# Performance work log

Hardware: AMD Instinct MI355X
Metric: run time of the kernel (lower is better)

The kernel has to match this reference:

```python
import jax, jax.numpy as jnp
import numpy as np

CONF_THRES = 0.8
NMS_THRES = 0.4
MAX_DET = 300          # fixed capacity for jit-compatible NMS output
N_BOXES = 262144
N_CLASSES = 80


def xywh2xyxy(x):
    xy, wh = x[..., :2], x[..., 2:4]
    return jnp.concatenate([xy - wh * 0.5, xy + wh * 0.5], axis=-1)


def bbox_iou(box, boxes):
    # one box [4] vs many [N,4]; original uses the +1 pixel-area convention
    x1 = jnp.maximum(box[0], boxes[:, 0])
    y1 = jnp.maximum(box[1], boxes[:, 1])
    x2 = jnp.minimum(box[2], boxes[:, 2])
    y2 = jnp.minimum(box[3], boxes[:, 3])
    inter = jnp.clip(x2 - x1 + 1, 0) * jnp.clip(y2 - y1 + 1, 0)
    a1 = (box[2] - box[0] + 1) * (box[3] - box[1] + 1)
    a2 = (boxes[:, 2] - boxes[:, 0] + 1) * (boxes[:, 3] - boxes[:, 1] + 1)
    return inter / (a1 + a2 - inter + 1e-16)


def nms_single(pred):
    # pred: [N, 85] raw YOLO output for one image
    boxes = xywh2xyxy(pred[:, :4])
    obj = pred[:, 4]
    cls_scores = pred[:, 5:]
    class_conf = cls_scores.max(axis=-1)
    class_pred = jnp.argmax(cls_scores, axis=-1).astype(pred.dtype)
    valid = obj >= CONF_THRES
    score = obj * class_conf
    # sort valid boxes by descending score; invalid pushed to the end
    order = jnp.argsort(jnp.where(valid, -score, jnp.inf))
    det = jnp.concatenate(
        [boxes, obj[:, None], class_conf[:, None], class_pred[:, None]], axis=1
    )[order]  # [N, 7] = x1,y1,x2,y2,obj,class_conf,class_pred
    valid = valid[order]

    def step(valid, _):
        idx = jnp.argmax(valid)            # first still-valid (= highest score)
        any_valid = jnp.any(valid)
        cur = det[idx]
        iou = bbox_iou(cur[:4], det[:, :4])
        invalid = (iou > NMS_THRES) & (det[:, 6] == cur[6]) & valid
        # weighted box merge over the suppressed group (as in original NMS)
        w = jnp.where(invalid, det[:, 4], 0.0)
        merged = (w[:, None] * det[:, :4]).sum(0) / (w.sum() + 1e-16)
        out = jnp.where(any_valid,
                        jnp.concatenate([merged, cur[4:]]),
                        jnp.zeros(7, pred.dtype))
        return valid & ~invalid, (out, any_valid)

    _, (kept, kept_valid) = jax.lax.scan(step, valid, None, length=MAX_DET)
    return kept, kept_valid  # [MAX_DET,7], [MAX_DET]


def setup_inputs() -> dict:
    key = jax.random.key(0)
    detections = jax.random.uniform(key, (1, N_BOXES, 5 + N_CLASSES), dtype=jnp.float32)
    return {"detections": detections}


def reference(detections):
    kept, kv = nms_single(detections[0])
    d = kept[:, 5:]                        # [MAX_DET, 2] = (class_conf, class_pred)
    conf_key = jnp.where(kv, d[:, 0], -jnp.inf)  # padded rows sort to the end
    order = jnp.argsort(conf_key)          # ascending (torch argsort)
    d = d[order][::-1]                     # torch.flip -> descending class_conf
    kv = kv[order][::-1]
    probs = jnp.where(kv, d[:, 0], 0.0)    # self.probs
    ids = d[:, 1][None, :]                 # self.ids, shape [1, MAX_DET]
    return ids, probs
```

## Files before the change

kernel.cpp:

```cpp
#include <hip/hip_runtime.h>

#pragma clang fp contract(off)

#define NBOX 262144
#define NCLS 80
#define ROWS 85
#define CAP 1024
#define NSUB 8
#define SUBCAP 128
#define POOL 8192
#define BPT 2
#define S1BOX 512

typedef unsigned long long ull;

__global__ __launch_bounds__(1024) void k_init(int* __restrict__ cnt_pad,
                                               int* __restrict__ pool_count) {
    const int t = threadIdx.x;
    for (int i = t; i < NCLS * NSUB * 16; i += 1024) cnt_pad[i] = 0;
    if (t == 0) *pool_count = 0;
}

__global__ __launch_bounds__(256) void k_stage1(const float* __restrict__ det,
                                                int* __restrict__ cnt_pad,
                                                ull* __restrict__ key2,
                                                float* __restrict__ conf2,
                                                float4* __restrict__ box2) {
    __shared__ int s_wl[S1BOX];
    __shared__ float s_obj[S1BOX];
    __shared__ int s_nv;
    const int t = threadIdx.x;
    const int b0 = blockIdx.x * S1BOX;
    const int sb = blockIdx.x & (NSUB - 1);

    if (t == 0) s_nv = 0;
    __syncthreads();

    float obj[BPT];
    #pragma unroll
    for (int i = 0; i < BPT; i++)
        obj[i] = det[(size_t)(b0 + (i << 8) + t) * ROWS + 4];
    #pragma unroll
    for (int i = 0; i < BPT; i++) {
        if (obj[i] >= 0.8f) {
            int r = atomicAdd(&s_nv, 1);
            s_wl[r] = (i << 8) + t;
            s_obj[r] = obj[i];
        }
    }
    __syncthreads();
    const int nv = s_nv;

    const int grp = t >> 4, c = t & 15;
    const int lane = t & 63;
    #pragma unroll 2
    for (int r0 = 0; r0 < nv; r0 += 16) {
        int widx = r0 + grp;
        if (widx < nv) {
            int b = s_wl[widx];
            const float* p = det + (size_t)(b0 + b) * ROWS;
            float aux = (c < 5) ? p[c] : 0.0f;
            float v0 = p[5 + c];
            float v1 = p[21 + c];
            float v2 = p[37 + c];
            float v3 = p[53 + c];
            float v4 = p[69 + c];
            float mv = v0; int mj = c;
            if (v1 > mv) { mv = v1; mj = 16 + c; }
            if (v2 > mv) { mv = v2; mj = 32 + c; }
            if (v3 > mv) { mv = v3; mj = 48 + c; }
            if (v4 > mv) { mv = v4; mj = 64 + c; }
            #pragma unroll
            for (int off = 8; off; off >>= 1) {
                float ov = __shfl_xor(mv, off);
                int oj = __shfl_xor(mj, off);
                if (ov > mv || (ov == mv && oj < mj)) { mv = ov; mj = oj; }
            }
            int gb = lane & 48;
            float x = __shfl(aux, gb + 0);
            float y = __shfl(aux, gb + 1);
            float w = __shfl(aux, gb + 2);
            float h = __shfl(aux, gb + 3);
            if (c == 0) {
                float ob = s_obj[widx];
                float score = ob * mv;
                float hw = w * 0.5f, hh = h * 0.5f;
                int gi = b0 + b;
                int r = atomicAdd(&cnt_pad[((mj * NSUB + sb) << 4)], 1);
                if (r < SUBCAP) {
                    int pos = (mj << 10) + (sb << 7) + r;
                    key2[pos] = ((ull)(~__float_as_uint(score)) << 32) | (unsigned)gi;
                    conf2[pos] = mv;
                    box2[pos] = make_float4(x - hw, y - hh, x + hw, y + hh);
                }
            }
        }
    }
}

template <int L>
__device__ __forceinline__ int exact_alive(ull (&k)[L]) {
    int a = 0;
    #pragma unroll
    for (int j = 0; j < L; j++) a += (int)__popcll(__ballot(k[j] != ~0ULL));
    return a;
}

template <int L>
__device__ __forceinline__ void pick_loop(ull (&k)[L], float4 (&bx)[L], float (&cf)[L],
                                          float (&ar)[L],
                                          int lane, int& alive, int& np,
                                          ull* pkey, float* pconf, int stopAt) {
    while (alive > stopAt && np < 300) {
        ull lm = k[0]; int lj = 0;
        #pragma unroll
        for (int j = 1; j < L; j++) if (k[j] < lm) { lm = k[j]; lj = j; }
        ull gm = lm;
        #pragma unroll
        for (int off = 32; off; off >>= 1) { ull o = __shfl_xor(gm, off); if (o < gm) gm = o; }
        if (gm == ~0ULL) { alive = 0; break; }
        float4 cb = bx[0]; float cc = cf[0];
        #pragma unroll
        for (int j = 1; j < L; j++) if (j == lj) { cb = bx[j]; cc = cf[j]; }
        ull wb = __ballot(lm == gm);
        int wl2 = (int)__ffsll((long long)wb) - 1;
        cb.x = __shfl(cb.x, wl2); cb.y = __shfl(cb.y, wl2);
        cb.z = __shfl(cb.z, wl2); cb.w = __shfl(cb.w, wl2);
        cc = __shfl(cc, wl2);
        if (lane == 0) { pkey[np] = gm; pconf[np] = cc; }
        np++;
        float a1 = (cb.z - cb.x + 1.0f) * (cb.w - cb.y + 1.0f);
        #pragma unroll
        for (int j = 0; j < L; j++) {
            if (k[j] != ~0ULL) {
                float4 b = bx[j];
                float xx1 = fmaxf(cb.x, b.x), yy1 = fmaxf(cb.y, b.y);
                float xx2 = fminf(cb.z, b.z), yy2 = fminf(cb.w, b.w);
                float iw = xx2 - xx1 + 1.0f, ih = yy2 - yy1 + 1.0f;
                float inter = fmaxf(iw, 0.0f) * fmaxf(ih, 0.0f);
                float iou = inter / (a1 + ar[j] - inter + 1e-16f);
                if (iou > 0.4f) k[j] = ~0ULL;
            }
        }
        if ((np & 7) == 0) alive = exact_alive(k);
    }
}

template <int LF, int LT>
__device__ __forceinline__ void compact_regs(ull (&k)[LF], float4 (&bx)[LF], float (&cf)[LF],
                                             ull (&k2)[LT], float4 (&b2)[LT], float (&c2)[LT],
                                             float (&a2)[LT],
                                             int lane, int alive,
                                             ull* dk, float4* db, float* dc) {
    int ci = 0;
    #pragma unroll
    for (int j = 0; j < LF; j++) if (k[j] != ~0ULL) ci++;
    int inc = ci;
    for (int off = 1; off < 64; off <<= 1) {
        int o = __shfl_up(inc, off);
        if (lane >= off) inc += o;
    }
    int wp = inc - ci;
    #pragma unroll
    for (int j = 0; j < LF; j++)
        if (k[j] != ~0ULL) { dk[wp] = k[j]; db[wp] = bx[j]; dc[wp] = cf[j]; wp++; }
    #pragma unroll
    for (int j = 0; j < LT; j++) {
        int pos = lane + (j << 6);
        bool ok = pos < alive;
        k2[j] = ok ? dk[pos] : ~0ULL;
        b2[j] = ok ? db[pos] : make_float4(0.f, 0.f, 0.f, 0.f);
        c2[j] = ok ? dc[pos] : 0.0f;
        a2[j] = (b2[j].z - b2[j].x + 1.0f) * (b2[j].w - b2[j].y + 1.0f);
    }
}

__global__ __launch_bounds__(64) void k_nms(const int* __restrict__ cnt_pad,
                                            const ull* __restrict__ key2,
                                            const float* __restrict__ conf2,
                                            const float4* __restrict__ box2,
                                            ull* __restrict__ pool_key,
                                            float* __restrict__ pool_conf,
                                            int* __restrict__ pool_cls,
                                            int* __restrict__ pool_count) {
    __shared__ ull sk[CAP];
    __shared__ float4 sbx[CAP];
    __shared__ float scf[CAP];
    __shared__ ull pkey[CAP];
    __shared__ float pconf[CAP];
    const int c = blockIdx.x, lane = threadIdx.x;
    const int s0 = c << 10;

    int cv0 = 0;
    if (lane < NSUB) cv0 = min(cnt_pad[((c * NSUB + lane) << 4)], SUBCAP);
    int ntot = cv0;
    #pragma unroll
    for (int off = 32; off; off >>= 1) ntot += __shfl_xor(ntot, off);

    ull k16[16]; float4 b16[16]; float c16[16]; float a16[16];
    #pragma unroll
    for (int j = 0; j < 16; j++) {
        int pos = lane + (j << 6);
        int sub = pos >> 7;
        int lim = __shfl(cv0, sub);
        bool ok = (pos & (SUBCAP - 1)) < lim;
        k16[j] = ok ? key2[s0 + pos] : ~0ULL;
        b16[j] = ok ? box2[s0 + pos] : make_float4(0.f, 0.f, 0.f, 0.f);
        c16[j] = ok ? conf2[s0 + pos] : 0.0f;
        a16[j] = (b16[j].z - b16[j].x + 1.0f) * (b16[j].w - b16[j].y + 1.0f);
    }
    int alive = ntot, np = 0;
    pick_loop<16>(k16, b16, c16, a16, lane, alive, np, pkey, pconf, 256);
    alive = exact_alive(k16);
    ull k4[4]; float4 b4[4]; float c4[4]; float a4[4];
    compact_regs<16, 4>(k16, b16, c16, k4, b4, c4, a4, lane, alive, sk, sbx, scf);
    pick_loop<4>(k4, b4, c4, a4, lane, alive, np, pkey, pconf, 64);
    alive = exact_alive(k4);
    ull k1[1]; float4 b1[1]; float c1[1]; float a1r[1];
    compact_regs<4, 1>(k4, b4, c4, k1, b1, c1, a1r, lane, alive, sk, sbx, scf);
    pick_loop<1>(k1, b1, c1, a1r, lane, alive, np, pkey, pconf, 0);

    int npw = min(np, 300);
    int base = 0;
    if (lane == 0 && npw) base = atomicAdd(pool_count, npw);
    base = __shfl(base, 0);
    for (int j = lane; j < npw; j += 64) {
        int pp = base + j;
        if (pp < POOL) {
            ull gm = pkey[j];
            pool_key[pp] = ((ull)((unsigned)(gm >> 32) & 0x7FFFFFFFu) << 32)
                         | ((gm & 0xFFFFFFFFull) << 14) | (ull)pp;
            pool_conf[pp] = pconf[j];
            pool_cls[pp] = c;
        }
    }
}

__device__ __forceinline__ void bsort512(ull (&x)[8], int lane) {
    #pragma unroll
    for (int k = 2; k <= 512; k <<= 1) {
        #pragma unroll
        for (int j = k >> 1; j >= 64; j >>= 1) {
            const int jr = j >> 6;
            #pragma unroll
            for (int r2 = 0; r2 < 8; r2++) {
                if ((r2 & jr) == 0) {
                    const bool asc = (((r2 << 6) & k) == 0);
                    ull a = x[r2], b = x[r2 | jr];
                    if ((a > b) == asc) { x[r2] = b; x[r2 | jr] = a; }
                }
            }
        }
        #pragma unroll
        for (int j = ((k >> 1) > 32 ? 32 : (k >> 1)); j >= 1; j >>= 1) {
            #pragma unroll
            for (int r2 = 0; r2 < 8; r2++) {
                int i = (r2 << 6) + lane;
                bool asc = ((i & k) == 0);
                ull o = __shfl_xor(x[r2], j);
                bool lower = ((lane & j) == 0);
                ull mn = x[r2] < o ? x[r2] : o;
                ull mx2 = x[r2] < o ? o : x[r2];
                x[r2] = (asc == lower) ? mn : mx2;
            }
        }
    }
}

__global__ __launch_bounds__(256) void k_final(const ull* __restrict__ pool_key,
                                               const float* __restrict__ pool_conf,
                                               const int* __restrict__ pool_cls,
                                               const int* __restrict__ pool_count,
                                               float* __restrict__ out) {
    __shared__ int s_hist[256];
    __shared__ int s_wt[4];
    __shared__ int s_stat[4];
    __shared__ ull s_buf[512];
    __shared__ unsigned s_cb[512];
    __shared__ unsigned s_cl[512];
    const int t = threadIdx.x, wave = t >> 6, lane = t & 63;
    const int K = min(*pool_count, POOL);
    ull key[32];
    #pragma unroll
    for (int j = 0; j < 32; j++) {
        int pos = t + (j << 8);
        key[j] = (pos < K) ? pool_key[pos] : ~0ULL;
    }

    const bool selAll = (K <= 511);
    int sh = 55;
    ull pfin = 0;
    if (!selAll) {
        ull p = 0;
        int gBelow = 0, r = 300;
        while (true) {
            s_hist[t] = 0;
            __syncthreads();
            #pragma unroll
            for (int j = 0; j < 32; j++) {
                ull kk = key[j];
                if ((kk >> (sh + 8)) == p)
                    atomicAdd(&s_hist[(int)((kk >> sh) & 0xFFull)], 1);
            }
            __syncthreads();
            int v = s_hist[t];
            int incv = v;
            for (int off = 1; off < 64; off <<= 1) {
                int o = __shfl_up(incv, off);
                if (lane >= off) incv += o;
            }
            if (lane == 63) s_wt[wave] = incv;
            __syncthreads();
            int wo = 0;
            #pragma unroll
            for (int w2 = 0; w2 < 4; w2++) if (w2 < wave) wo += s_wt[w2];
            int cumIncl = wo + incv;
            int cumExcl = cumIncl - v;
            if (cumExcl < r && r <= cumIncl) {
                s_stat[0] = t; s_stat[1] = cumExcl; s_stat[2] = cumIncl;
            }
            __syncthreads();
            int D = s_stat[0], below = s_stat[1], incl = s_stat[2];
            if (gBelow + incl <= 511 || sh == 7) {
                pfin = (p << 8) | (ull)D;
                break;
            }
            p = (p << 8) | (ull)D;
            gBelow += below;
            r = 300 - gBelow;
            sh -= 8;
            __syncthreads();
        }
    }

    if (t == 0) s_stat[3] = 0;
    __syncthreads();
    int ci = 0;
    #pragma unroll
    for (int j = 0; j < 32; j++) {
        ull kk = key[j];
        bool sel = selAll ? ((kk >> 63) == 0) : ((kk >> sh) <= pfin);
        if (sel) ci++;
    }
    int inc = ci;
    for (int off = 1; off < 64; off <<= 1) {
        int o = __shfl_up(inc, off);
        if (lane >= off) inc += o;
    }
    int wtot = __shfl(inc, 63);
    int wbase2 = 0;
    if (lane == 0 && wtot) wbase2 = atomicAdd(&s_stat[3], wtot);
    wbase2 = __shfl(wbase2, 0);
    int wp = wbase2 + inc - ci;
    #pragma unroll
    for (int j = 0; j < 32; j++) {
        ull kk = key[j];
        bool sel = selAll ? ((kk >> 63) == 0) : ((kk >> sh) <= pfin);
        if (sel) s_buf[wp++] = kk;
    }
    __syncthreads();
    const int S = s_stat[3];
    for (int i = t; i < 512; i += 256) if (i >= S) s_buf[i] = ~0ULL;
    __syncthreads();
    if (wave != 0) return;

    #pragma clang loop unroll(disable)
    for (int pass = 0; pass < 2; pass++) {
        ull x[8];
        #pragma unroll
        for (int r2 = 0; r2 < 8; r2++) x[r2] = s_buf[(r2 << 6) + lane];
        bsort512(x, lane);
        if (pass == 0) {
            #pragma unroll
            for (int r2 = 0; r2 < 8; r2++) {
                int i = (r2 << 6) + lane;
                ull kk = x[r2];
                ull k2 = ~0ULL;
                if (i < 300 && kk != ~0ULL) {
                    int pidx = (int)(kk & 0x3FFFull);
                    unsigned cb = __float_as_uint(pool_conf[pidx]);
                    unsigned cl = (unsigned)pool_cls[pidx];
                    s_cb[i] = cb; s_cl[i] = cl;
                    k2 = ((ull)(~cb) << 32) | (unsigned)(~i);
                }
                s_buf[i] = k2;
            }
        } else {
            #pragma unroll
            for (int r2 = 0; r2 < 8; r2++) {
                int i = (r2 << 6) + lane;
                if (i < 300) {
                    ull kk = x[r2];
                    float idv = 0.0f, pv = 0.0f;
                    if (kk != ~0ULL) {
                        int slot = (int)(~(unsigned)(kk & 0xFFFFFFFFull));
                        pv = __uint_as_float(s_cb[slot]);
                        idv = (float)(int)s_cl[slot];
                    }
                    out[i] = idv;
                    out[300 + i] = pv;
                }
            }
        }
    }
}

extern "C" void kernel_launch(void* const* d_in, const int* in_sizes, int n_in,
                              void* d_out, int out_size, void* d_ws, size_t ws_size,
                              hipStream_t stream) {
    const float* det = (const float*)d_in[0];
    float* out = (float*)d_out;
    char* ws = (char*)d_ws;

    int* cnt_pad = (int*)(ws + 0);
    int* pool_count = (int*)(ws + 40960);
    ull* key2 = (ull*)(ws + 41024);
    float* conf2 = (float*)(ws + 696384);
    float4* box2 = (float4*)(ws + 1024064);
    ull* pool_key = (ull*)(ws + 2334784);
    float* pool_conf = (float*)(ws + 2400320);
    int* pool_cls = (int*)(ws + 2433088);

    k_init<<<1, 1024, 0, stream>>>(cnt_pad, pool_count);
    k_stage1<<<NBOX / S1BOX, 256, 0, stream>>>(det, cnt_pad, key2, conf2, box2);
    k_nms<<<NCLS, 64, 0, stream>>>(cnt_pad, key2, conf2, box2,
                                   pool_key, pool_conf, pool_cls, pool_count);
    k_final<<<1, 256, 0, stream>>>(pool_key, pool_conf, pool_cls, pool_count, out);
}
```

Before: 182.7 us.

## Fuse per-class NMS and final top-k into one kernel via last-block ticket

Merges the per-class NMS kernel and the single-block final selection kernel into one launch. Each of the 80 blocks runs NMS on wave 0, publishes its pool entries with agent-scope atomic stores, then takes a ticket from a done counter, and only the last block performs the final selection and sort. This removes one kernel launch and the inter-kernel gap. In exchange, every NMS block now launches 256 threads and allocates the final-stage shared memory, which may reduce occupancy, and correctness depends on the relaxed atomics plus waitcnt giving enough memory ordering.

Result: no change. 181.7 us (-0.5%).

```diff
diff --git a/kernel.cpp b/kernel.cpp
--- a/kernel.cpp
+++ b/kernel.cpp
@@ -15,10 +15,11 @@
 typedef unsigned long long ull;
 
 __global__ __launch_bounds__(1024) void k_init(int* __restrict__ cnt_pad,
-                                               int* __restrict__ pool_count) {
+                                               int* __restrict__ pool_count,
+                                               int* __restrict__ done_count) {
     const int t = threadIdx.x;
     for (int i = t; i < NCLS * NSUB * 16; i += 1024) cnt_pad[i] = 0;
-    if (t == 0) *pool_count = 0;
+    if (t == 0) { *pool_count = 0; *done_count = 0; }
 }
 
 __global__ __launch_bounds__(256) void k_stage1(const float* __restrict__ det,
@@ -175,67 +176,6 @@
     }
 }
 
-__global__ __launch_bounds__(64) void k_nms(const int* __restrict__ cnt_pad,
-                                            const ull* __restrict__ key2,
-                                            const float* __restrict__ conf2,
-                                            const float4* __restrict__ box2,
-                                            ull* __restrict__ pool_key,
-                                            float* __restrict__ pool_conf,
-                                            int* __restrict__ pool_cls,
-                                            int* __restrict__ pool_count) {
-    __shared__ ull sk[CAP];
-    __shared__ float4 sbx[CAP];
-    __shared__ float scf[CAP];
-    __shared__ ull pkey[CAP];
-    __shared__ float pconf[CAP];
-    const int c = blockIdx.x, lane = threadIdx.x;
-    const int s0 = c << 10;
-
-    int cv0 = 0;
-    if (lane < NSUB) cv0 = min(cnt_pad[((c * NSUB + lane) << 4)], SUBCAP);
-    int ntot = cv0;
-    #pragma unroll
-    for (int off = 32; off; off >>= 1) ntot += __shfl_xor(ntot, off);
-
-    ull k16[16]; float4 b16[16]; float c16[16]; float a16[16];
-    #pragma unroll
-    for (int j = 0; j < 16; j++) {
-        int pos = lane + (j << 6);
-        int sub = pos >> 7;
-        int lim = __shfl(cv0, sub);
-        bool ok = (pos & (SUBCAP - 1)) < lim;
-        k16[j] = ok ? key2[s0 + pos] : ~0ULL;
-        b16[j] = ok ? box2[s0 + pos] : make_float4(0.f, 0.f, 0.f, 0.f);
-        c16[j] = ok ? conf2[s0 + pos] : 0.0f;
-        a16[j] = (b16[j].z - b16[j].x + 1.0f) * (b16[j].w - b16[j].y + 1.0f);
-    }
-    int alive = ntot, np = 0;
-    pick_loop<16>(k16, b16, c16, a16, lane, alive, np, pkey, pconf, 256);
-    alive = exact_alive(k16);
-    ull k4[4]; float4 b4[4]; float c4[4]; float a4[4];
-    compact_regs<16, 4>(k16, b16, c16, k4, b4, c4, a4, lane, alive, sk, sbx, scf);
-    pick_loop<4>(k4, b4, c4, a4, lane, alive, np, pkey, pconf, 64);
-    alive = exact_alive(k4);
-    ull k1[1]; float4 b1[1]; float c1[1]; float a1r[1];
-    compact_regs<4, 1>(k4, b4, c4, k1, b1, c1, a1r, lane, alive, sk, sbx, scf);
-    pick_loop<1>(k1, b1, c1, a1r, lane, alive, np, pkey, pconf, 0);
-
-    int npw = min(np, 300);
-    int base = 0;
-    if (lane == 0 && npw) base = atomicAdd(pool_count, npw);
-    base = __shfl(base, 0);
-    for (int j = lane; j < npw; j += 64) {
-        int pp = base + j;
-        if (pp < POOL) {
-            ull gm = pkey[j];
-            pool_key[pp] = ((ull)((unsigned)(gm >> 32) & 0x7FFFFFFFu) << 32)
-                         | ((gm & 0xFFFFFFFFull) << 14) | (ull)pp;
-            pool_conf[pp] = pconf[j];
-            pool_cls[pp] = c;
-        }
-    }
-}
-
 __device__ __forceinline__ void bsort512(ull (&x)[8], int lane) {
     #pragma unroll
     for (int k = 2; k <= 512; k <<= 1) {
@@ -267,24 +207,99 @@
     }
 }
 
-__global__ __launch_bounds__(256) void k_final(const ull* __restrict__ pool_key,
-                                               const float* __restrict__ pool_conf,
-                                               const int* __restrict__ pool_cls,
-                                               const int* __restrict__ pool_count,
-                                               float* __restrict__ out) {
+__global__ __launch_bounds__(256) void k_nmsfinal(const int* __restrict__ cnt_pad,
+                                                  const ull* __restrict__ key2,
+                                                  const float* __restrict__ conf2,
+                                                  const float4* __restrict__ box2,
+                                                  ull* __restrict__ pool_key,
+                                                  float* __restrict__ pool_conf,
+                                                  int* __restrict__ pool_cls,
+                                                  int* __restrict__ pool_count,
+                                                  int* __restrict__ done_count,
+                                                  float* __restrict__ out) {
+    __shared__ ull sk[CAP];
+    __shared__ float4 sbx[CAP];
+    __shared__ float scf[CAP];
+    __shared__ ull pkey[CAP];
+    __shared__ float pconf[CAP];
+    __shared__ int s_fin;
     __shared__ int s_hist[256];
     __shared__ int s_wt[4];
     __shared__ int s_stat[4];
     __shared__ ull s_buf[512];
     __shared__ unsigned s_cb[512];
     __shared__ unsigned s_cl[512];
-    const int t = threadIdx.x, wave = t >> 6, lane = t & 63;
-    const int K = min(*pool_count, POOL);
+
+    const int c = blockIdx.x, t = threadIdx.x, lane = t & 63, wave = t >> 6;
+
+    if (wave == 0) {
+        const int s0 = c << 10;
+        int cv0 = 0;
+        if (lane < NSUB) cv0 = min(cnt_pad[((c * NSUB + lane) << 4)], SUBCAP);
+        int ntot = cv0;
+        #pragma unroll
+        for (int off = 32; off; off >>= 1) ntot += __shfl_xor(ntot, off);
+
+        ull k16[16]; float4 b16[16]; float c16[16]; float a16[16];
+        #pragma unroll
+        for (int j = 0; j < 16; j++) {
+            int pos = lane + (j << 6);
+            int sub = pos >> 7;
+            int lim = __shfl(cv0, sub);
+            bool ok = (pos & (SUBCAP - 1)) < lim;
+            k16[j] = ok ? key2[s0 + pos] : ~0ULL;
+            b16[j] = ok ? box2[s0 + pos] : make_float4(0.f, 0.f, 0.f, 0.f);
+            c16[j] = ok ? conf2[s0 + pos] : 0.0f;
+            a16[j] = (b16[j].z - b16[j].x + 1.0f) * (b16[j].w - b16[j].y + 1.0f);
+        }
+        int alive = ntot, np = 0;
+        pick_loop<16>(k16, b16, c16, a16, lane, alive, np, pkey, pconf, 256);
+        alive = exact_alive(k16);
+        ull k4[4]; float4 b4[4]; float c4[4]; float a4[4];
+        compact_regs<16, 4>(k16, b16, c16, k4, b4, c4, a4, lane, alive, sk, sbx, scf);
+        pick_loop<4>(k4, b4, c4, a4, lane, alive, np, pkey, pconf, 64);
+        alive = exact_alive(k4);
+        ull k1[1]; float4 b1[1]; float c1[1]; float a1r[1];
+        compact_regs<4, 1>(k4, b4, c4, k1, b1, c1, a1r, lane, alive, sk, sbx, scf);
+        pick_loop<1>(k1, b1, c1, a1r, lane, alive, np, pkey, pconf, 0);
+
+        int npw = min(np, 300);
+        int base = 0;
+        if (lane == 0 && npw) base = atomicAdd(pool_count, npw);
+        base = __shfl(base, 0);
+        for (int j = lane; j < npw; j += 64) {
+            int pp = base + j;
+            if (pp < POOL) {
+                ull gm = pkey[j];
+                ull pk = ((ull)((unsigned)(gm >> 32) & 0x7FFFFFFFu) << 32)
+                       | ((gm & 0xFFFFFFFFull) << 14) | (ull)pp;
+                __hip_atomic_store(&pool_key[pp], pk,
+                                   __ATOMIC_RELAXED, __HIP_MEMORY_SCOPE_AGENT);
+                __hip_atomic_store(&pool_conf[pp], pconf[j],
+                                   __ATOMIC_RELAXED, __HIP_MEMORY_SCOPE_AGENT);
+                __hip_atomic_store(&pool_cls[pp], c,
+                                   __ATOMIC_RELAXED, __HIP_MEMORY_SCOPE_AGENT);
+            }
+        }
+        asm volatile("s_waitcnt vmcnt(0)" ::: "memory");
+    }
+    __syncthreads();
+    if (t == 0) {
+        int ticket = atomicAdd(done_count, 1);
+        s_fin = (ticket == NCLS - 1) ? 1 : 0;
+    }
+    __syncthreads();
+    if (!s_fin) return;
+
+    const int K = min(__hip_atomic_load(pool_count, __ATOMIC_RELAXED,
+                                        __HIP_MEMORY_SCOPE_AGENT), POOL);
     ull key[32];
     #pragma unroll
     for (int j = 0; j < 32; j++) {
         int pos = t + (j << 8);
-        key[j] = (pos < K) ? pool_key[pos] : ~0ULL;
+        key[j] = (pos < K) ? __hip_atomic_load(&pool_key[pos], __ATOMIC_RELAXED,
+                                               __HIP_MEMORY_SCOPE_AGENT)
+                           : ~0ULL;
     }
 
     const bool selAll = (K <= 511);
@@ -378,8 +393,11 @@
                 ull k2 = ~0ULL;
                 if (i < 300 && kk != ~0ULL) {
                     int pidx = (int)(kk & 0x3FFFull);
-                    unsigned cb = __float_as_uint(pool_conf[pidx]);
-                    unsigned cl = (unsigned)pool_cls[pidx];
+                    unsigned cb = __float_as_uint(
+                        __hip_atomic_load(&pool_conf[pidx], __ATOMIC_RELAXED,
+                                          __HIP_MEMORY_SCOPE_AGENT));
+                    unsigned cl = (unsigned)__hip_atomic_load(&pool_cls[pidx],
+                                          __ATOMIC_RELAXED, __HIP_MEMORY_SCOPE_AGENT);
                     s_cb[i] = cb; s_cl[i] = cl;
                     k2 = ((ull)(~cb) << 32) | (unsigned)(~i);
                 }
@@ -414,6 +432,7 @@
 
     int* cnt_pad = (int*)(ws + 0);
     int* pool_count = (int*)(ws + 40960);
+    int* done_count = (int*)(ws + 40964);
     ull* key2 = (ull*)(ws + 41024);
     float* conf2 = (float*)(ws + 696384);
     float4* box2 = (float4*)(ws + 1024064);
@@ -421,9 +440,9 @@
     float* pool_conf = (float*)(ws + 2400320);
     int* pool_cls = (int*)(ws + 2433088);
 
-    k_init<<<1, 1024, 0, stream>>>(cnt_pad, pool_count);
+    k_init<<<1, 1024, 0, stream>>>(cnt_pad, pool_count, done_count);
     k_stage1<<<NBOX / S1BOX, 256, 0, stream>>>(det, cnt_pad, key2, conf2, box2);
-    k_nms<<<NCLS, 64, 0, stream>>>(cnt_pad, key2, conf2, box2,
-                                   pool_key, pool_conf, pool_cls, pool_count);
-    k_final<<<1, 256, 0, stream>>>(pool_key, pool_conf, pool_cls, pool_count, out);
-}
+    k_nmsfinal<<<NCLS, 256, 0, stream>>>(cnt_pad, key2, conf2, box2,
+                                         pool_key, pool_conf, pool_cls, pool_count,
+                                         done_count, out);
+}
```
